# Kernel tuning notes

Hardware: AMD Instinct MI355X
Metric: run time of the kernel (lower is better)

The kernel has to match this reference:

```python
import jax, jax.numpy as jnp
import numpy as np

K1, K2 = 3, 3
DIL = 1
PAD = (DIL * (K1 - 1) // 2, DIL * (K2 - 1) // 2)


def _unfold(x, k1, k2, dilation, padding):
    # x: [B, C, H, W] -> patches [B, C, k1*k2, H*W], matching F.unfold ordering
    B, C, H, W = x.shape
    p0, p1 = padding
    xp = jnp.pad(x, ((0, 0), (0, 0), (p0, p0), (p1, p1)))
    cols = []
    for i in range(k1):  # small fixed loop over kernel taps
        for j in range(k2):
            cols.append(xp[:, :, i * dilation:i * dilation + H, j * dilation:j * dilation + W])
    patches = jnp.stack(cols, axis=2)  # [B, C, k1*k2, H, W]
    return patches.reshape(B, C, k1 * k2, H * W)


def setup_inputs() -> dict:
    key = jax.random.key(0)
    k1, k2, k3, k4 = jax.random.split(key, 4)
    B, Cin, Cout, H, W = 32, 128, 128, 32, 32
    x = jax.random.normal(k1, (B, Cin, H, W), dtype=jnp.float32)
    mask = jax.random.uniform(k2, (1, K1 * K2, H * W), dtype=jnp.float32)
    weight = jax.random.normal(k3, (Cout, Cin, K1, K2), dtype=jnp.float32) * 0.05
    bias = jax.random.normal(k4, (Cout,), dtype=jnp.float32) * 0.05
    return {"x": x, "mask": mask, "weight": weight, "bias": bias}


def reference(x, mask, weight, bias):
    B, Cin, H, W = x.shape
    Cout = weight.shape[0]
    KK = K1 * K2
    # unfold -> [B, Cin, KK, L]
    patches = _unfold(x, K1, K2, DIL, PAD)
    # per-patch mask multiply (mask broadcasts over B and Cin): mask [1, KK, L]
    patches = patches * mask[:, None, :, :]  # [B, Cin, KK, L]
    # dense matmul with flattened weight [Cout, Cin*KK]
    wm = weight.reshape(Cout, Cin * KK)
    out = jnp.einsum('ok,bkl->bol', wm, patches.reshape(B, Cin * KK, H * W))
    out = out + bias[None, :, None]
    return out.reshape(B, Cout, H, W)
```

## Files before the change

kernel.cpp:

```cpp
#include <hip/hip_runtime.h>
#include <hip/hip_fp16.h>

typedef _Float16 half8 __attribute__((ext_vector_type(8)));
typedef _Float16 half4 __attribute__((ext_vector_type(4)));
typedef float f32x4 __attribute__((ext_vector_type(4)));

#define CIN   128
#define COUT  128
#define HH    32
#define WW    32
#define LTOT  1024
#define KKT   9
#define KDIM  1152

#define SMEM_BYTES 69632

__global__ void prep_w_kernel(const float* __restrict__ w, _Float16* __restrict__ wt) {
  int i = blockIdx.x * 256 + threadIdx.x;
  int q = i >> 10;
  int o = (i >> 3) & 127;
  int j = i & 7;
  int kk = q >> 4;
  int c  = ((q & 15) << 3) + j;
  wt[i] = (_Float16)w[(o * CIN + c) * KKT + kk];
}

__global__ __launch_bounds__(512, 1)
void conv_mfma_kernel(const float* __restrict__ x,
                      const _Float16* __restrict__ wt,
                      const float* __restrict__ mask,
                      const float* __restrict__ bias,
                      float* __restrict__ out) {
  extern __shared__ char smem[];
  const int tid = threadIdx.x;
  int bid = blockIdx.x;
  bid = (bid & 7) * 32 + (bid >> 3);
  const int b  = bid >> 3;
  const int l0 = (bid & 7) << 7;
  const int h0 = (bid & 7) << 2;

  const int lane = tid & 63, wid = tid >> 6;
  const int lr = lane & 15, lg = lane >> 4;
  const int kh = wid >> 2;
  const int wq = wid & 3;
  const int mw = (wq >> 1) << 6;
  const int nw = (wq & 1) << 6;

  half4 mvh[9];
  {
    const float* mr = mask + l0 + nw + lr;
#pragma unroll
    for (int kk = 0; kk < 9; ++kk) {
#pragma unroll
      for (int nj = 0; nj < 4; ++nj) mvh[kk][nj] = (_Float16)mr[kk * LTOT + nj * 16];
    }
  }

  const int wv = tid & 31, q16 = tid >> 5;
  char* bdst = smem + wv * 256 + ((q16 ^ (wv & 15)) << 4);
  const float* xb = x + (size_t)b * CIN * LTOT;
  {
    float fr[6][8];
#pragma unroll
    for (int r = 0; r < 6; ++r) {
      const int hg = h0 - 1 + r;
      if ((unsigned)hg < (unsigned)HH) {
        const float* s = xb + (size_t)q16 * 8 * LTOT + hg * WW + wv;
#pragma unroll
        for (int j = 0; j < 8; ++j) fr[r][j] = s[(size_t)j * LTOT];
      }
    }
    asm volatile("s_waitcnt vmcnt(0)" ::: "memory");
#pragma unroll
    for (int r = 0; r < 6; ++r) {
      const int hg = h0 - 1 + r;
      half8 v = (half8){0, 0, 0, 0, 0, 0, 0, 0};
      if ((unsigned)hg < (unsigned)HH) {
#pragma unroll
        for (int j = 0; j < 8; ++j) v[j] = (_Float16)fr[r][j];
      }
      *(half8*)(bdst + r * 8192) = v;
    }
  }
  __syncthreads();

  const char* abase = (const char*)wt + lg * 2048 + (mw + lr) * 16;

  f32x4 acc[4][4];
#pragma unroll
  for (int mi = 0; mi < 4; ++mi)
#pragma unroll
    for (int nj = 0; nj < 4; ++nj)
      acc[mi][nj] = (f32x4){0.f, 0.f, 0.f, 0.f};

  half8 apf[20][4];
  auto loadA = [&](int s) {
    const int kk = s >> 1, hs = s & 1;
    const int qb = kk * 16 + (kh * 2 + hs) * 4;
    const char* ab = abase + qb * 2048;
    apf[s][0] = *(const half8*)(ab);
    apf[s][1] = *(const half8*)(ab + 256);
    apf[s][2] = *(const half8*)(ab + 512);
    apf[s][3] = *(const half8*)(ab + 768);
  };
  loadA(0);
  loadA(1);

#pragma unroll
  for (int s = 0; s < 18; ++s) {
    if (s + 2 < 18) loadA(s + 2);

    const int kk = s >> 1, hs = s & 1;
    const int di = (kk * 11) >> 5;
    const int dj = kk - 3 * di;
    const int qb = kk * 16 + (kh * 2 + hs) * 4;
    const int q15 = (qb + lg) & 15;

    half8 bfr[4];
#pragma unroll
    for (int nj = 0; nj < 4; ++nj) {
      const int wb = ((nj & 1) << 4) + lr + dj - 1;
      const bool vld = (unsigned)wb < (unsigned)WW;
      const int wc = vld ? wb : 0;
      const int hrow = (nw >> 5) + (nj >> 1) + di;
      const _Float16 mh = vld ? mvh[kk][nj] : (_Float16)0.f;
      bfr[nj] = *(const half8*)(smem + hrow * 8192 + wc * 256 +
                                ((q15 ^ (wc & 15)) << 4)) * mh;
    }

    __builtin_amdgcn_s_setprio(1);
    acc[0][0] = __builtin_amdgcn_mfma_f32_16x16x32_f16(apf[s][0], bfr[0], acc[0][0], 0, 0, 0);
    acc[1][0] = __builtin_amdgcn_mfma_f32_16x16x32_f16(apf[s][1], bfr[0], acc[1][0], 0, 0, 0);
    acc[2][0] = __builtin_amdgcn_mfma_f32_16x16x32_f16(apf[s][2], bfr[0], acc[2][0], 0, 0, 0);
    acc[3][0] = __builtin_amdgcn_mfma_f32_16x16x32_f16(apf[s][3], bfr[0], acc[3][0], 0, 0, 0);
    acc[0][1] = __builtin_amdgcn_mfma_f32_16x16x32_f16(apf[s][0], bfr[1], acc[0][1], 0, 0, 0);
    acc[1][1] = __builtin_amdgcn_mfma_f32_16x16x32_f16(apf[s][1], bfr[1], acc[1][1], 0, 0, 0);
    acc[2][1] = __builtin_amdgcn_mfma_f32_16x16x32_f16(apf[s][2], bfr[1], acc[2][1], 0, 0, 0);
    acc[3][1] = __builtin_amdgcn_mfma_f32_16x16x32_f16(apf[s][3], bfr[1], acc[3][1], 0, 0, 0);
    acc[0][2] = __builtin_amdgcn_mfma_f32_16x16x32_f16(apf[s][0], bfr[2], acc[0][2], 0, 0, 0);
    acc[1][2] = __builtin_amdgcn_mfma_f32_16x16x32_f16(apf[s][1], bfr[2], acc[1][2], 0, 0, 0);
    acc[2][2] = __builtin_amdgcn_mfma_f32_16x16x32_f16(apf[s][2], bfr[2], acc[2][2], 0, 0, 0);
    acc[3][2] = __builtin_amdgcn_mfma_f32_16x16x32_f16(apf[s][3], bfr[2], acc[3][2], 0, 0, 0);
    acc[0][3] = __builtin_amdgcn_mfma_f32_16x16x32_f16(apf[s][0], bfr[3], acc[0][3], 0, 0, 0);
    acc[1][3] = __builtin_amdgcn_mfma_f32_16x16x32_f16(apf[s][1], bfr[3], acc[1][3], 0, 0, 0);
    acc[2][3] = __builtin_amdgcn_mfma_f32_16x16x32_f16(apf[s][2], bfr[3], acc[2][3], 0, 0, 0);
    acc[3][3] = __builtin_amdgcn_mfma_f32_16x16x32_f16(apf[s][3], bfr[3], acc[3][3], 0, 0, 0);
    __builtin_amdgcn_s_setprio(0);
  }

  __syncthreads();
  char* red = smem + wq * 17408 + lane * 272;
  if (kh == 1) {
#pragma unroll
    for (int mi = 0; mi < 4; ++mi)
#pragma unroll
      for (int nj = 0; nj < 4; ++nj)
        *(f32x4*)(red + (mi * 4 + nj) * 16) = acc[mi][nj];
  }
  __syncthreads();

  if (kh == 0) {
#pragma unroll
    for (int mi = 0; mi < 4; ++mi)
#pragma unroll
      for (int nj = 0; nj < 4; ++nj) {
        f32x4 p = *(const f32x4*)(red + (mi * 4 + nj) * 16);
        acc[mi][nj].x += p.x; acc[mi][nj].y += p.y;
        acc[mi][nj].z += p.z; acc[mi][nj].w += p.w;
      }

    float* outb = out + (size_t)b * COUT * LTOT + l0;
#pragma unroll
    for (int mi = 0; mi < 4; ++mi) {
#pragma unroll
      for (int rr = 0; rr < 4; ++rr) {
        const int o = mw + mi * 16 + lg * 4 + rr;
        const float bv = bias[o];
        float* orow = outb + (size_t)o * LTOT + nw + lr;
#pragma unroll
        for (int nj = 0; nj < 4; ++nj)
          orow[nj * 16] = acc[mi][nj][rr] + bv;
      }
    }
  }
}

extern "C" void kernel_launch(void* const* d_in, const int* in_sizes, int n_in,
                              void* d_out, int out_size, void* d_ws, size_t ws_size,
                              hipStream_t stream) {
  const float* x    = (const float*)d_in[0];
  const float* mask = (const float*)d_in[1];
  const float* w    = (const float*)d_in[2];
  const float* bias = (const float*)d_in[3];
  float* out = (float*)d_out;
  _Float16* wt = (_Float16*)d_ws;

  (void)hipFuncSetAttribute(reinterpret_cast<const void*>(conv_mfma_kernel),
                            hipFuncAttributeMaxDynamicSharedMemorySize, SMEM_BYTES);

  prep_w_kernel<<<576, 256, 0, stream>>>(w, wt);
  conv_mfma_kernel<<<256, 512, SMEM_BYTES, stream>>>(x, wt, mask, bias, out);
}
```

Before: 27.16 us.

## Halve spatial tile per block, double grid, drop A prefetch for higher occupancy

Each block now covers 64 output positions (2 image rows) instead of 128, so the grid doubles to 512 blocks and LDS usage drops to 32 KB. The launch bound moves to 4 blocks per CU. The 20-stage register prefetch of the weight fragments is removed in favour of direct loads each step, which cuts register pressure so more waves can be resident. The trade-off is that each weight fragment now feeds half as many MFMAs, the halo overhead per block grows, and weight-load latency is no longer hidden by software prefetch.

```diff
diff --git a/kernel.cpp b/kernel.cpp
--- a/kernel.cpp
+++ b/kernel.cpp
@@ -2,7 +2,6 @@
 #include <hip/hip_fp16.h>
 
 typedef _Float16 half8 __attribute__((ext_vector_type(8)));
-typedef _Float16 half4 __attribute__((ext_vector_type(4)));
 typedef float f32x4 __attribute__((ext_vector_type(4)));
 
 #define CIN   128
@@ -13,7 +12,7 @@
 #define KKT   9
 #define KDIM  1152
 
-#define SMEM_BYTES 69632
+#define SMEM_BYTES 32768
 
 __global__ void prep_w_kernel(const float* __restrict__ w, _Float16* __restrict__ wt) {
   int i = blockIdx.x * 256 + threadIdx.x;
@@ -25,7 +24,7 @@
   wt[i] = (_Float16)w[(o * CIN + c) * KKT + kk];
 }
 
-__global__ __launch_bounds__(512, 1)
+__global__ __launch_bounds__(512, 4)
 void conv_mfma_kernel(const float* __restrict__ x,
                       const _Float16* __restrict__ wt,
                       const float* __restrict__ mask,
@@ -34,35 +33,37 @@
   extern __shared__ char smem[];
   const int tid = threadIdx.x;
   int bid = blockIdx.x;
-  bid = (bid & 7) * 32 + (bid >> 3);
-  const int b  = bid >> 3;
-  const int l0 = (bid & 7) << 7;
-  const int h0 = (bid & 7) << 2;
+  bid = (bid & 7) * 64 + (bid >> 3);
+  const int b  = bid >> 4;
+  const int lq = bid & 15;
+  const int l0 = lq << 6;
+  const int h0 = lq << 1;
 
   const int lane = tid & 63, wid = tid >> 6;
   const int lr = lane & 15, lg = lane >> 4;
   const int kh = wid >> 2;
   const int wq = wid & 3;
   const int mw = (wq >> 1) << 6;
-  const int nw = (wq & 1) << 6;
+  const int nw = (wq & 1) << 5;
+  const int hl = nw >> 5;
 
-  half4 mvh[9];
+  _Float16 mvh[9][2];
   {
     const float* mr = mask + l0 + nw + lr;
 #pragma unroll
-    for (int kk = 0; kk < 9; ++kk) {
+    for (int kk = 0; kk < 9; ++kk)
 #pragma unroll
-      for (int nj = 0; nj < 4; ++nj) mvh[kk][nj] = (_Float16)mr[kk * LTOT + nj * 16];
-    }
+      for (int nj = 0; nj < 2; ++nj)
+        mvh[kk][nj] = (_Float16)mr[kk * LTOT + nj * 16];
   }
 
   const int wv = tid & 31, q16 = tid >> 5;
   char* bdst = smem + wv * 256 + ((q16 ^ (wv & 15)) << 4);
   const float* xb = x + (size_t)b * CIN * LTOT;
   {
-    float fr[6][8];
+    float fr[4][8];
 #pragma unroll
-    for (int r = 0; r < 6; ++r) {
+    for (int r = 0; r < 4; ++r) {
       const int hg = h0 - 1 + r;
       if ((unsigned)hg < (unsigned)HH) {
         const float* s = xb + (size_t)q16 * 8 * LTOT + hg * WW + wv;
@@ -72,7 +73,7 @@
     }
     asm volatile("s_waitcnt vmcnt(0)" ::: "memory");
 #pragma unroll
-    for (int r = 0; r < 6; ++r) {
+    for (int r = 0; r < 4; ++r) {
       const int hg = h0 - 1 + r;
       half8 v = (half8){0, 0, 0, 0, 0, 0, 0, 0};
       if ((unsigned)hg < (unsigned)HH) {
@@ -86,76 +87,59 @@
 
   const char* abase = (const char*)wt + lg * 2048 + (mw + lr) * 16;
 
-  f32x4 acc[4][4];
+  f32x4 acc[4][2];
 #pragma unroll
   for (int mi = 0; mi < 4; ++mi)
 #pragma unroll
-    for (int nj = 0; nj < 4; ++nj)
+    for (int nj = 0; nj < 2; ++nj)
       acc[mi][nj] = (f32x4){0.f, 0.f, 0.f, 0.f};
-
-  half8 apf[20][4];
-  auto loadA = [&](int s) {
-    const int kk = s >> 1, hs = s & 1;
-    const int qb = kk * 16 + (kh * 2 + hs) * 4;
-    const char* ab = abase + qb * 2048;
-    apf[s][0] = *(const half8*)(ab);
-    apf[s][1] = *(const half8*)(ab + 256);
-    apf[s][2] = *(const half8*)(ab + 512);
-    apf[s][3] = *(const half8*)(ab + 768);
-  };
-  loadA(0);
-  loadA(1);
 
 #pragma unroll
   for (int s = 0; s < 18; ++s) {
-    if (s + 2 < 18) loadA(s + 2);
-
     const int kk = s >> 1, hs = s & 1;
     const int di = (kk * 11) >> 5;
     const int dj = kk - 3 * di;
     const int qb = kk * 16 + (kh * 2 + hs) * 4;
     const int q15 = (qb + lg) & 15;
+    const char* ab = abase + qb * 2048;
 
-    half8 bfr[4];
+    half8 a0 = *(const half8*)(ab);
+    half8 a1 = *(const half8*)(ab + 256);
+    half8 a2 = *(const half8*)(ab + 512);
+    half8 a3 = *(const half8*)(ab + 768);
+
+    half8 bfr[2];
 #pragma unroll
-    for (int nj = 0; nj < 4; ++nj) {
-      const int wb = ((nj & 1) << 4) + lr + dj - 1;
+    for (int nj = 0; nj < 2; ++nj) {
+      const int wb = (nj << 4) + lr + dj - 1;
       const bool vld = (unsigned)wb < (unsigned)WW;
       const int wc = vld ? wb : 0;
-      const int hrow = (nw >> 5) + (nj >> 1) + di;
+      const int hrow = hl + di;
       const _Float16 mh = vld ? mvh[kk][nj] : (_Float16)0.f;
       bfr[nj] = *(const half8*)(smem + hrow * 8192 + wc * 256 +
                                 ((q15 ^ (wc & 15)) << 4)) * mh;
     }
 
     __builtin_amdgcn_s_setprio(1);
-    acc[0][0] = __builtin_amdgcn_mfma_f32_16x16x32_f16(apf[s][0], bfr[0], acc[0][0], 0, 0, 0);
-    acc[1][0] = __builtin_amdgcn_mfma_f32_16x16x32_f16(apf[s][1], bfr[0], acc[1][0], 0, 0, 0);
-    acc[2][0] = __builtin_amdgcn_mfma_f32_16x16x32_f16(apf[s][2], bfr[0], acc[2][0], 0, 0, 0);
-    acc[3][0] = __builtin_amdgcn_mfma_f32_16x16x32_f16(apf[s][3], bfr[0], acc[3][0], 0, 0, 0);
-    acc[0][1] = __builtin_amdgcn_mfma_f32_16x16x32_f16(apf[s][0], bfr[1], acc[0][1], 0, 0, 0);
-    acc[1][1] = __builtin_amdgcn_mfma_f32_16x16x32_f16(apf[s][1], bfr[1], acc[1][1], 0, 0, 0);
-    acc[2][1] = __builtin_amdgcn_mfma_f32_16x16x32_f16(apf[s][2], bfr[1], acc[2][1], 0, 0, 0);
-    acc[3][1] = __builtin_amdgcn_mfma_f32_16x16x32_f16(apf[s][3], bfr[1], acc[3][1], 0, 0, 0);
-    acc[0][2] = __builtin_amdgcn_mfma_f32_16x16x32_f16(apf[s][0], bfr[2], acc[0][2], 0, 0, 0);
-    acc[1][2] = __builtin_amdgcn_mfma_f32_16x16x32_f16(apf[s][1], bfr[2], acc[1][2], 0, 0, 0);
-    acc[2][2] = __builtin_amdgcn_mfma_f32_16x16x32_f16(apf[s][2], bfr[2], acc[2][2], 0, 0, 0);
-    acc[3][2] = __builtin_amdgcn_mfma_f32_16x16x32_f16(apf[s][3], bfr[2], acc[3][2], 0, 0, 0);
-    acc[0][3] = __builtin_amdgcn_mfma_f32_16x16x32_f16(apf[s][0], bfr[3], acc[0][3], 0, 0, 0);
-    acc[1][3] = __builtin_amdgcn_mfma_f32_16x16x32_f16(apf[s][1], bfr[3], acc[1][3], 0, 0, 0);
-    acc[2][3] = __builtin_amdgcn_mfma_f32_16x16x32_f16(apf[s][2], bfr[3], acc[2][3], 0, 0, 0);
-    acc[3][3] = __builtin_amdgcn_mfma_f32_16x16x32_f16(apf[s][3], bfr[3], acc[3][3], 0, 0, 0);
+    acc[0][0] = __builtin_amdgcn_mfma_f32_16x16x32_f16(a0, bfr[0], acc[0][0], 0, 0, 0);
+    acc[1][0] = __builtin_amdgcn_mfma_f32_16x16x32_f16(a1, bfr[0], acc[1][0], 0, 0, 0);
+    acc[2][0] = __builtin_amdgcn_mfma_f32_16x16x32_f16(a2, bfr[0], acc[2][0], 0, 0, 0);
+    acc[3][0] = __builtin_amdgcn_mfma_f32_16x16x32_f16(a3, bfr[0], acc[3][0], 0, 0, 0);
+    acc[0][1] = __builtin_amdgcn_mfma_f32_16x16x32_f16(a0, bfr[1], acc[0][1], 0, 0, 0);
+    acc[1][1] = __builtin_amdgcn_mfma_f32_16x16x32_f16(a1, bfr[1], acc[1][1], 0, 0, 0);
+    acc[2][1] = __builtin_amdgcn_mfma_f32_16x16x32_f16(a2, bfr[1], acc[2][1], 0, 0, 0);
+    acc[3][1] = __builtin_amdgcn_mfma_f32_16x16x32_f16(a3, bfr[1], acc[3][1], 0, 0, 0);
     __builtin_amdgcn_s_setprio(0);
   }
 
   __syncthreads();
-  char* red = smem + wq * 17408 + lane * 272;
+  char* red = smem + wq * 8192 + lane * 128;
   if (kh == 1) {
 #pragma unroll
     for (int mi = 0; mi < 4; ++mi)
 #pragma unroll
-      for (int nj = 0; nj < 4; ++nj)
-        *(f32x4*)(red + (mi * 4 + nj) * 16) = acc[mi][nj];
+      for (int nj = 0; nj < 2; ++nj)
+        *(f32x4*)(red + (mi * 2 + nj) * 16) = acc[mi][nj];
   }
   __syncthreads();
 
@@ -163,8 +147,8 @@
 #pragma unroll
     for (int mi = 0; mi < 4; ++mi)
 #pragma unroll
-      for (int nj = 0; nj < 4; ++nj) {
-        f32x4 p = *(const f32x4*)(red + (mi * 4 + nj) * 16);
+      for (int nj = 0; nj < 2; ++nj) {
+        f32x4 p = *(const f32x4*)(red + (mi * 2 + nj) * 16);
         acc[mi][nj].x += p.x; acc[mi][nj].y += p.y;
         acc[mi][nj].z += p.z; acc[mi][nj].w += p.w;
       }
@@ -178,7 +162,7 @@
         const float bv = bias[o];
         float* orow = outb + (size_t)o * LTOT + nw + lr;
 #pragma unroll
-        for (int nj = 0; nj < 4; ++nj)
+        for (int nj = 0; nj < 2; ++nj)
           orow[nj * 16] = acc[mi][nj][rr] + bv;
       }
     }
@@ -199,5 +183,5 @@
                             hipFuncAttributeMaxDynamicSharedMemorySize, SMEM_BYTES);
 
   prep_w_kernel<<<576, 256, 0, stream>>>(w, wt);
-  conv_mfma_kernel<<<256, 512, SMEM_BYTES, stream>>>(x, wt, mask, bias, out);
+  conv_mfma_kernel<<<512, 512, SMEM_BYTES, stream>>>(x, wt, mask, bias, out);
 }
```

New measurement: 27.46 us. About the same (+1.1%).
